# Kernel optimization log

Hardware: AMD Instinct MI355X
Metric: run time of the kernel (lower is better)

Reference implementation:

```python
import jax, jax.numpy as jnp
import numpy as np

B, N, D, H = 256, 1000, 256, 8
DH = D // H
NEG = -1e9
TANH_CLIP = 10.0


def setup_inputs() -> dict:
    key = jax.random.key(0)
    ks = jax.random.split(key, 16)
    f = jax.random.normal
    return {
        "node_embeddings": f(ks[0], (B, N, D), jnp.float32),
        "graph_context": f(ks[1], (B, D), jnp.float32),
        "glimpse_key": f(ks[2], (B, H, N, DH), jnp.float32),
        "glimpse_val": f(ks[3], (B, H, N, DH), jnp.float32),
        "logit_key": f(ks[4], (B, N, D), jnp.float32),
        "capacity": jax.random.uniform(ks[5], (B, 1, 1), jnp.float32),
        "remaining_demand": jax.random.uniform(ks[6], (B, 1, 1), jnp.float32),
        "remaining_nodes": jax.random.uniform(ks[7], (B, 1, 1), jnp.float32),
        "W_ctx": f(ks[8], (2 * D + 3, 2 * D), jnp.float32) / np.sqrt(2 * D + 3),
        "W_out": f(ks[9], (D, D), jnp.float32) / np.sqrt(D),
        "W_sa": f(ks[10], (D, D), jnp.float32) / np.sqrt(D),
        "head": jax.random.randint(ks[11], (B,), 0, N),
        "feasible_nodes": jax.random.randint(ks[12], (B, N), 0, 2, dtype=jnp.int32),
    }


def _mha(q, k, v, mask):
    # q: [B,H,1,DH]; k,v: [B,H,N,DH]; mask: [B,N] True = feasible
    scores = jnp.einsum('bhqd,bhnd->bhqn', q, k) / np.sqrt(DH)
    scores = jnp.where(mask[:, None, None, :], scores, NEG)
    attn = jax.nn.softmax(scores, axis=-1)
    out = jnp.einsum('bhqn,bhnd->bhqd', attn, v)  # [B,H,1,DH]
    return out.transpose(0, 2, 1, 3).reshape(out.shape[0], D)  # [B,D]


def reference(node_embeddings, graph_context, glimpse_key, glimpse_val,
              logit_key, capacity, remaining_demand, remaining_nodes,
              W_ctx, W_out, W_sa, head, feasible_nodes):
    mask = feasible_nodes.astype(bool)
    no_feasible = ~jnp.any(mask, axis=-1)
    mask = mask.at[:, 0].set(mask[:, 0] | no_feasible)  # force node 0 feasible if all masked

    # dynamic features: [B,3]
    dyn = jnp.concatenate([capacity[:, 0], remaining_demand[:, 0], remaining_nodes[:, 0]], axis=-1)
    # current head node embedding via gather_by_index: [B,D]
    cur = jnp.take_along_axis(node_embeddings, head[:, None, None], axis=1)[:, 0]
    step_context = jnp.concatenate([cur, graph_context, dyn], axis=-1) @ W_ctx  # [B,2D]
    glimpse_q, head_in = step_context[:, :D], step_context[:, D:]

    # glimpse multi-head attention (q_len = 1)
    qh = glimpse_q.reshape(B, 1, H, DH).transpose(0, 2, 1, 3)
    glimpse = _mha(qh, glimpse_key, glimpse_val, mask) @ W_out  # [B,D]

    # single-head pointer logits + tanh clip + masking + log-softmax
    logits = jnp.einsum('bd,bnd->bn', glimpse, logit_key) / np.sqrt(D)
    logits = TANH_CLIP * jnp.tanh(logits)
    logits = jnp.where(mask, logits, NEG)
    log_p = jax.nn.log_softmax(logits, axis=-1)  # [B,N]

    # SimpleSetAttention head encoding over the same cached K/V
    qh2 = head_in.reshape(B, 1, H, DH).transpose(0, 2, 1, 3)
    head_encoding = _mha(qh2, glimpse_key, glimpse_val, mask) @ W_sa  # [B,D]
    return log_p, head_encoding
```

## Files before the change

kernel.cpp:

```cpp
#include <hip/hip_runtime.h>
#include <math.h>

#define B 256
#define N 1000
#define D 256
#define H 8
#define DH 32
#define NEG (-1000000000.0f)

__device__ __forceinline__ float waveReduceMax(float v) {
#pragma unroll
    for (int off = 32; off >= 1; off >>= 1) v = fmaxf(v, __shfl_xor(v, off, 64));
    return v;
}
__device__ __forceinline__ float waveReduceSum(float v) {
#pragma unroll
    for (int off = 32; off >= 1; off >>= 1) v += __shfl_xor(v, off, 64);
    return v;
}

__global__ __launch_bounds__(256) void k_mask(
    const int* __restrict__ feas, int* __restrict__ mask_ws)
{
    __shared__ int sRed[4];
    const int b = blockIdx.x;
    const int tid = threadIdx.x;
    int vals[4];
    int orloc = 0;
#pragma unroll
    for (int k = 0; k < 4; ++k) {
        int n = tid + k * 256;
        int v = (n < N) ? feas[b * N + n] : 0;
        vals[k] = v;
        orloc |= v;
    }
#pragma unroll
    for (int off = 32; off >= 1; off >>= 1) orloc |= __shfl_xor(orloc, off, 64);
    if ((tid & 63) == 0) sRed[tid >> 6] = orloc;
    __syncthreads();
    const int anyf = sRed[0] | sRed[1] | sRed[2] | sRed[3];
#pragma unroll
    for (int k = 0; k < 4; ++k) {
        int n = tid + k * 256;
        if (n < N) {
            int m = vals[k];
            if (n == 0 && !anyf) m = 1;
            mask_ws[b * N + n] = m;
        }
    }
}

__global__ __launch_bounds__(256) void k_ctx(
    const float* __restrict__ ne, const float* __restrict__ gc,
    const float* __restrict__ cap, const float* __restrict__ dem,
    const float* __restrict__ rem, const float* __restrict__ Wctx,
    const int* __restrict__ head,
    float* __restrict__ q1_ws, float* __restrict__ q2_ws)
{
    __shared__ float xs[515];
    const int tid = threadIdx.x;
    const int b = blockIdx.x >> 1;
    const int half = blockIdx.x & 1;
    const int hd = head[b];
    for (int i = tid; i < 515; i += 256) {
        float v;
        if (i < 256)       v = ne[(size_t)(b * N + hd) * D + i];
        else if (i < 512)  v = gc[b * D + (i - 256)];
        else if (i == 512) v = cap[b];
        else if (i == 513) v = dem[b];
        else               v = rem[b];
        xs[i] = v;
    }
    __syncthreads();
    const float* __restrict__ wcol = Wctx + half * 256 + tid;
    float a0 = 0.f, a1 = 0.f, a2 = 0.f, a3 = 0.f;
    int i = 0;
#pragma unroll 2
    for (; i + 4 <= 515; i += 4) {
        a0 = fmaf(xs[i + 0], wcol[(i + 0) * 512], a0);
        a1 = fmaf(xs[i + 1], wcol[(i + 1) * 512], a1);
        a2 = fmaf(xs[i + 2], wcol[(i + 2) * 512], a2);
        a3 = fmaf(xs[i + 3], wcol[(i + 3) * 512], a3);
    }
    for (; i < 515; ++i) a0 = fmaf(xs[i], wcol[i * 512], a0);
    float a = (a0 + a1) + (a2 + a3);
    (half ? q2_ws : q1_ws)[b * D + tid] = a;
}

__global__ __launch_bounds__(256) void k_attn(
    const float* __restrict__ gk, const float* __restrict__ gv,
    const float* __restrict__ q1_ws, const float* __restrict__ q2_ws,
    const int* __restrict__ mask_ws,
    float* __restrict__ out1_ws, float* __restrict__ out2_ws)
{
    __shared__ float s1[N];
    __shared__ float s2[N];
    __shared__ float redA[4], redB[4];
    __shared__ __align__(16) float part1[4][DH];
    __shared__ __align__(16) float part2[4][DH];

    const int tid = threadIdx.x;
    const int b = blockIdx.x >> 3;
    const int h = blockIdx.x & 7;
    const int wid = tid >> 6;
    const int lane = tid & 63;
    const int nsub = lane >> 3;
    const int d4 = lane & 7;

    const float4 q1v = ((const float4*)(q1_ws + (size_t)b * D + h * DH))[d4];
    const float4 q2v = ((const float4*)(q2_ws + (size_t)b * D + h * DH))[d4];
    const float scale = 0.17677669529663687f;
    const float4* __restrict__ kb = (const float4*)(gk + (size_t)(b * H + h) * N * DH);
    const int rbase = wid * 32 + nsub;

#pragma unroll 2
    for (int base = 0; base < 896; base += 128) {
        float4 kv[4];
#pragma unroll
        for (int k = 0; k < 4; ++k) kv[k] = kb[(base + rbase + k * 8) * 8 + d4];
#pragma unroll
        for (int k = 0; k < 4; ++k) {
            float d1 = kv[k].x * q1v.x + kv[k].y * q1v.y + kv[k].z * q1v.z + kv[k].w * q1v.w;
            float d2 = kv[k].x * q2v.x + kv[k].y * q2v.y + kv[k].z * q2v.z + kv[k].w * q2v.w;
            d1 += __shfl_xor(d1, 1, 64); d1 += __shfl_xor(d1, 2, 64); d1 += __shfl_xor(d1, 4, 64);
            d2 += __shfl_xor(d2, 1, 64); d2 += __shfl_xor(d2, 2, 64); d2 += __shfl_xor(d2, 4, 64);
            if (d4 == 0) {
                int r = base + rbase + k * 8;
                s1[r] = d1 * scale;
                s2[r] = d2 * scale;
            }
        }
    }
    {
        float4 kv[4];
        int rr[4];
#pragma unroll
        for (int k = 0; k < 4; ++k) {
            rr[k] = 896 + rbase + k * 8;
            kv[k] = (rr[k] < N) ? kb[rr[k] * 8 + d4] : make_float4(0.f, 0.f, 0.f, 0.f);
        }
#pragma unroll
        for (int k = 0; k < 4; ++k) {
            float d1 = kv[k].x * q1v.x + kv[k].y * q1v.y + kv[k].z * q1v.z + kv[k].w * q1v.w;
            float d2 = kv[k].x * q2v.x + kv[k].y * q2v.y + kv[k].z * q2v.z + kv[k].w * q2v.w;
            d1 += __shfl_xor(d1, 1, 64); d1 += __shfl_xor(d1, 2, 64); d1 += __shfl_xor(d1, 4, 64);
            d2 += __shfl_xor(d2, 1, 64); d2 += __shfl_xor(d2, 2, 64); d2 += __shfl_xor(d2, 4, 64);
            if (d4 == 0 && rr[k] < N) {
                s1[rr[k]] = d1 * scale;
                s2[rr[k]] = d2 * scale;
            }
        }
    }
    __syncthreads();

    float m1 = -INFINITY, m2 = -INFINITY;
    float v1[4], v2[4];
#pragma unroll
    for (int k = 0; k < 4; ++k) {
        int n = tid + k * 256;
        if (n < N) {
            int mm = mask_ws[b * N + n];
            v1[k] = mm ? s1[n] : NEG;
            v2[k] = mm ? s2[n] : NEG;
            m1 = fmaxf(m1, v1[k]);
            m2 = fmaxf(m2, v2[k]);
        } else { v1[k] = NEG; v2[k] = NEG; }
    }
    m1 = waveReduceMax(m1);
    m2 = waveReduceMax(m2);
    if ((tid & 63) == 0) { redA[wid] = m1; redB[wid] = m2; }
    __syncthreads();
    m1 = fmaxf(fmaxf(redA[0], redA[1]), fmaxf(redA[2], redA[3]));
    m2 = fmaxf(fmaxf(redB[0], redB[1]), fmaxf(redB[2], redB[3]));
    __syncthreads();

    float sum1 = 0.f, sum2 = 0.f;
#pragma unroll
    for (int k = 0; k < 4; ++k) {
        int n = tid + k * 256;
        if (n < N) {
            float e1 = __expf(v1[k] - m1);
            float e2 = __expf(v2[k] - m2);
            s1[n] = e1; s2[n] = e2;
            sum1 += e1; sum2 += e2;
        }
    }
    sum1 = waveReduceSum(sum1);
    sum2 = waveReduceSum(sum2);
    if ((tid & 63) == 0) { redA[wid] = sum1; redB[wid] = sum2; }
    __syncthreads();
    sum1 = redA[0] + redA[1] + redA[2] + redA[3];
    sum2 = redB[0] + redB[1] + redB[2] + redB[3];

    const float4* __restrict__ vb = (const float4*)(gv + (size_t)(b * H + h) * N * DH);
    float4 a1 = {0.f, 0.f, 0.f, 0.f}, a2 = {0.f, 0.f, 0.f, 0.f};
#pragma unroll 2
    for (int base = 0; base < 896; base += 128) {
        float4 vv[4];
#pragma unroll
        for (int k = 0; k < 4; ++k) vv[k] = vb[(base + rbase + k * 8) * 8 + d4];
#pragma unroll
        for (int k = 0; k < 4; ++k) {
            int r = base + rbase + k * 8;
            float p1 = s1[r], p2 = s2[r];
            a1.x = fmaf(p1, vv[k].x, a1.x); a1.y = fmaf(p1, vv[k].y, a1.y);
            a1.z = fmaf(p1, vv[k].z, a1.z); a1.w = fmaf(p1, vv[k].w, a1.w);
            a2.x = fmaf(p2, vv[k].x, a2.x); a2.y = fmaf(p2, vv[k].y, a2.y);
            a2.z = fmaf(p2, vv[k].z, a2.z); a2.w = fmaf(p2, vv[k].w, a2.w);
        }
    }
    {
        float4 vv[4];
        int rr[4];
#pragma unroll
        for (int k = 0; k < 4; ++k) {
            rr[k] = 896 + rbase + k * 8;
            vv[k] = (rr[k] < N) ? vb[rr[k] * 8 + d4] : make_float4(0.f, 0.f, 0.f, 0.f);
        }
#pragma unroll
        for (int k = 0; k < 4; ++k) {
            float p1 = (rr[k] < N) ? s1[rr[k]] : 0.f;
            float p2 = (rr[k] < N) ? s2[rr[k]] : 0.f;
            a1.x = fmaf(p1, vv[k].x, a1.x); a1.y = fmaf(p1, vv[k].y, a1.y);
            a1.z = fmaf(p1, vv[k].z, a1.z); a1.w = fmaf(p1, vv[k].w, a1.w);
            a2.x = fmaf(p2, vv[k].x, a2.x); a2.y = fmaf(p2, vv[k].y, a2.y);
            a2.z = fmaf(p2, vv[k].z, a2.z); a2.w = fmaf(p2, vv[k].w, a2.w);
        }
    }
#pragma unroll
    for (int off = 8; off <= 32; off <<= 1) {
        a1.x += __shfl_xor(a1.x, off, 64); a1.y += __shfl_xor(a1.y, off, 64);
        a1.z += __shfl_xor(a1.z, off, 64); a1.w += __shfl_xor(a1.w, off, 64);
        a2.x += __shfl_xor(a2.x, off, 64); a2.y += __shfl_xor(a2.y, off, 64);
        a2.z += __shfl_xor(a2.z, off, 64); a2.w += __shfl_xor(a2.w, off, 64);
    }
    if (lane < 8) {
        ((float4*)part1[wid])[d4] = a1;
        ((float4*)part2[wid])[d4] = a2;
    }
    __syncthreads();

    if (tid < 64) {
        int set = tid >> 5, d = tid & 31;
        float tot = set ? (part2[0][d] + part2[1][d] + part2[2][d] + part2[3][d])
                        : (part1[0][d] + part1[1][d] + part1[2][d] + part1[3][d]);
        float rs = 1.f / (set ? sum2 : sum1);
        (set ? out2_ws : out1_ws)[b * D + h * DH + d] = tot * rs;
    }
}

__global__ __launch_bounds__(256) void k_proj(
    const float* __restrict__ out1_ws, const float* __restrict__ out2_ws,
    const float* __restrict__ Wout, const float* __restrict__ Wsa,
    float* __restrict__ glimpse_ws, float* __restrict__ head_enc)
{
    __shared__ float x[D];
    const int tid = threadIdx.x;
    const int b = blockIdx.x >> 1;
    const int which = blockIdx.x & 1;
    const float* __restrict__ src = which ? out2_ws : out1_ws;
    x[tid] = src[b * D + tid];
    __syncthreads();
    const float* __restrict__ W = which ? Wsa : Wout;
    float a = 0.f;
#pragma unroll 8
    for (int i = 0; i < D; ++i) a = fmaf(x[i], W[i * D + tid], a);
    (which ? head_enc : glimpse_ws)[b * D + tid] = a;
}

__global__ __launch_bounds__(256) void k_logits(
    const float* __restrict__ lk, const float* __restrict__ glimpse_ws,
    const int* __restrict__ mask_ws, float* __restrict__ logits_ws)
{
    __shared__ __align__(16) float gsh[D];
    const int tid = threadIdx.x;
    const int b = blockIdx.x >> 2;
    const int chunk = blockIdx.x & 3;
    gsh[tid] = glimpse_ws[b * D + tid];
    __syncthreads();

    const int lane = tid & 63, wid = tid >> 6;
    const float4 gv = ((const float4*)gsh)[lane];
    const int n0 = chunk * 250;
    const int nend = n0 + 250;
    for (int n = n0 + wid * 4; n < nend; n += 16) {
        float4 kr[4];
#pragma unroll
        for (int j = 0; j < 4; ++j) {
            int nn = n + j;
            kr[j] = (nn < nend) ? ((const float4*)(lk + (size_t)(b * N + nn) * D))[lane]
                                : make_float4(0.f, 0.f, 0.f, 0.f);
        }
        float p[4];
#pragma unroll
        for (int j = 0; j < 4; ++j)
            p[j] = kr[j].x * gv.x + kr[j].y * gv.y + kr[j].z * gv.z + kr[j].w * gv.w;
#pragma unroll
        for (int off = 32; off >= 1; off >>= 1) {
#pragma unroll
            for (int j = 0; j < 4; ++j) p[j] += __shfl_xor(p[j], off, 64);
        }
        if (lane == 0) {
#pragma unroll
            for (int j = 0; j < 4; ++j) {
                int nn = n + j;
                if (nn < nend) {
                    float l = 10.0f * tanhf(p[j] * 0.0625f);
                    logits_ws[b * N + nn] = mask_ws[b * N + nn] ? l : NEG;
                }
            }
        }
    }
}

__global__ __launch_bounds__(256) void k_logsoftmax(
    const float* __restrict__ logits_ws, float* __restrict__ logp)
{
    __shared__ float red[4];
    const int tid = threadIdx.x;
    const int b = blockIdx.x;
    float v[4];
    float m = -INFINITY;
#pragma unroll
    for (int k = 0; k < 4; ++k) {
        int n = tid + k * 256;
        v[k] = (n < N) ? logits_ws[b * N + n] : -INFINITY;
        m = fmaxf(m, v[k]);
    }
    m = waveReduceMax(m);
    if ((tid & 63) == 0) red[tid >> 6] = m;
    __syncthreads();
    m = fmaxf(fmaxf(red[0], red[1]), fmaxf(red[2], red[3]));
    __syncthreads();
    float s = 0.f;
#pragma unroll
    for (int k = 0; k < 4; ++k) {
        int n = tid + k * 256;
        if (n < N) s += __expf(v[k] - m);
    }
    s = waveReduceSum(s);
    if ((tid & 63) == 0) red[tid >> 6] = s;
    __syncthreads();
    s = red[0] + red[1] + red[2] + red[3];
    const float lse = m + logf(s);
#pragma unroll
    for (int k = 0; k < 4; ++k) {
        int n = tid + k * 256;
        if (n < N) logp[b * N + n] = v[k] - lse;
    }
}

extern "C" void kernel_launch(void* const* d_in, const int* in_sizes, int n_in,
                              void* d_out, int out_size, void* d_ws, size_t ws_size,
                              hipStream_t stream) {
    const float* ne   = (const float*)d_in[0];
    const float* gc   = (const float*)d_in[1];
    const float* gk   = (const float*)d_in[2];
    const float* gvv  = (const float*)d_in[3];
    const float* lk   = (const float*)d_in[4];
    const float* cap  = (const float*)d_in[5];
    const float* dem  = (const float*)d_in[6];
    const float* rem  = (const float*)d_in[7];
    const float* Wctx = (const float*)d_in[8];
    const float* Wout = (const float*)d_in[9];
    const float* Wsa  = (const float*)d_in[10];
    const int*   head = (const int*)d_in[11];
    const int*   feas = (const int*)d_in[12];
    float* out = (float*)d_out;

    float* ws        = (float*)d_ws;
    float* q1_ws     = ws;
    float* q2_ws     = q1_ws + B * D;
    int*   mask_ws   = (int*)(q2_ws + B * D);
    float* out1_ws   = (float*)(mask_ws + B * N);
    float* out2_ws   = out1_ws + B * D;
    float* glimpse_ws= out2_ws + B * D;
    float* logits_ws = glimpse_ws + B * D;

    hipLaunchKernelGGL(k_mask, dim3(B), dim3(256), 0, stream, feas, mask_ws);
    hipLaunchKernelGGL(k_ctx, dim3(B * 2), dim3(256), 0, stream,
                       ne, gc, cap, dem, rem, Wctx, head, q1_ws, q2_ws);
    hipLaunchKernelGGL(k_attn, dim3(B * H), dim3(256), 0, stream,
                       gk, gvv, q1_ws, q2_ws, mask_ws, out1_ws, out2_ws);
    hipLaunchKernelGGL(k_proj, dim3(B * 2), dim3(256), 0, stream,
                       out1_ws, out2_ws, Wout, Wsa, glimpse_ws, out + B * N);
    hipLaunchKernelGGL(k_logits, dim3(B * 4), dim3(256), 0, stream,
                       lk, glimpse_ws, mask_ws, logits_ws);
    hipLaunchKernelGGL(k_logsoftmax, dim3(B), dim3(256), 0, stream,
                       logits_ws, out);
}
```

Baseline: 831.3 us.

## Use DPP/swizzle reductions and wider per-thread loads in attention and logits kernels

New measurement: 815.0 us. About the same (-2.0%).

```diff
diff --git a/kernel.cpp b/kernel.cpp
--- a/kernel.cpp
+++ b/kernel.cpp
@@ -17,6 +17,22 @@
 #pragma unroll
     for (int off = 32; off >= 1; off >>= 1) v += __shfl_xor(v, off, 64);
     return v;
+}
+
+__device__ __forceinline__ float qxor1_add(float v) {
+    int t = __builtin_amdgcn_update_dpp(0, __float_as_int(v), 0xB1, 0xF, 0xF, true);
+    return v + __int_as_float(t);
+}
+__device__ __forceinline__ float qxor2_add(float v) {
+    int t = __builtin_amdgcn_update_dpp(0, __float_as_int(v), 0x4E, 0xF, 0xF, true);
+    return v + __int_as_float(t);
+}
+__device__ __forceinline__ float sxor4_add(float v) {
+    int t = __builtin_amdgcn_ds_swizzle(__float_as_int(v), 0x101F);
+    return v + __int_as_float(t);
+}
+__device__ __forceinline__ float dot4(float4 a, float4 b) {
+    return a.x * b.x + a.y * b.y + a.z * b.z + a.w * b.w;
 }
 
 __global__ __launch_bounds__(256) void k_mask(
@@ -111,40 +127,40 @@
     const float4 q2v = ((const float4*)(q2_ws + (size_t)b * D + h * DH))[d4];
     const float scale = 0.17677669529663687f;
     const float4* __restrict__ kb = (const float4*)(gk + (size_t)(b * H + h) * N * DH);
-    const int rbase = wid * 32 + nsub;
-
-#pragma unroll 2
-    for (int base = 0; base < 896; base += 128) {
-        float4 kv[4];
-#pragma unroll
-        for (int k = 0; k < 4; ++k) kv[k] = kb[(base + rbase + k * 8) * 8 + d4];
-#pragma unroll
-        for (int k = 0; k < 4; ++k) {
-            float d1 = kv[k].x * q1v.x + kv[k].y * q1v.y + kv[k].z * q1v.z + kv[k].w * q1v.w;
-            float d2 = kv[k].x * q2v.x + kv[k].y * q2v.y + kv[k].z * q2v.z + kv[k].w * q2v.w;
-            d1 += __shfl_xor(d1, 1, 64); d1 += __shfl_xor(d1, 2, 64); d1 += __shfl_xor(d1, 4, 64);
-            d2 += __shfl_xor(d2, 1, 64); d2 += __shfl_xor(d2, 2, 64); d2 += __shfl_xor(d2, 4, 64);
+    const int rb8 = wid * 64 + nsub;
+
+#pragma unroll 1
+    for (int base = 0; base < 768; base += 256) {
+        float4 kv[8];
+#pragma unroll
+        for (int k = 0; k < 8; ++k) kv[k] = kb[(base + rb8 + k * 8) * 8 + d4];
+#pragma unroll
+        for (int k = 0; k < 8; ++k) {
+            float d1 = dot4(kv[k], q1v);
+            float d2 = dot4(kv[k], q2v);
+            d1 = qxor1_add(d1); d1 = qxor2_add(d1); d1 = sxor4_add(d1);
+            d2 = qxor1_add(d2); d2 = qxor2_add(d2); d2 = sxor4_add(d2);
             if (d4 == 0) {
-                int r = base + rbase + k * 8;
+                int r = base + rb8 + k * 8;
                 s1[r] = d1 * scale;
                 s2[r] = d2 * scale;
             }
         }
     }
     {
-        float4 kv[4];
-        int rr[4];
-#pragma unroll
-        for (int k = 0; k < 4; ++k) {
-            rr[k] = 896 + rbase + k * 8;
+        float4 kv[8];
+        int rr[8];
+#pragma unroll
+        for (int k = 0; k < 8; ++k) {
+            rr[k] = 768 + rb8 + k * 8;
             kv[k] = (rr[k] < N) ? kb[rr[k] * 8 + d4] : make_float4(0.f, 0.f, 0.f, 0.f);
         }
 #pragma unroll
-        for (int k = 0; k < 4; ++k) {
-            float d1 = kv[k].x * q1v.x + kv[k].y * q1v.y + kv[k].z * q1v.z + kv[k].w * q1v.w;
-            float d2 = kv[k].x * q2v.x + kv[k].y * q2v.y + kv[k].z * q2v.z + kv[k].w * q2v.w;
-            d1 += __shfl_xor(d1, 1, 64); d1 += __shfl_xor(d1, 2, 64); d1 += __shfl_xor(d1, 4, 64);
-            d2 += __shfl_xor(d2, 1, 64); d2 += __shfl_xor(d2, 2, 64); d2 += __shfl_xor(d2, 4, 64);
+        for (int k = 0; k < 8; ++k) {
+            float d1 = dot4(kv[k], q1v);
+            float d2 = dot4(kv[k], q2v);
+            d1 = qxor1_add(d1); d1 = qxor2_add(d1); d1 = sxor4_add(d1);
+            d2 = qxor1_add(d2); d2 = qxor2_add(d2); d2 = sxor4_add(d2);
             if (d4 == 0 && rr[k] < N) {
                 s1[rr[k]] = d1 * scale;
                 s2[rr[k]] = d2 * scale;
@@ -194,14 +210,14 @@
 
     const float4* __restrict__ vb = (const float4*)(gv + (size_t)(b * H + h) * N * DH);
     float4 a1 = {0.f, 0.f, 0.f, 0.f}, a2 = {0.f, 0.f, 0.f, 0.f};
-#pragma unroll 2
-    for (int base = 0; base < 896; base += 128) {
-        float4 vv[4];
-#pragma unroll
-        for (int k = 0; k < 4; ++k) vv[k] = vb[(base + rbase + k * 8) * 8 + d4];
-#pragma unroll
-        for (int k = 0; k < 4; ++k) {
-            int r = base + rbase + k * 8;
+#pragma unroll 1
+    for (int base = 0; base < 768; base += 256) {
+        float4 vv[8];
+#pragma unroll
+        for (int k = 0; k < 8; ++k) vv[k] = vb[(base + rb8 + k * 8) * 8 + d4];
+#pragma unroll
+        for (int k = 0; k < 8; ++k) {
+            int r = base + rb8 + k * 8;
             float p1 = s1[r], p2 = s2[r];
             a1.x = fmaf(p1, vv[k].x, a1.x); a1.y = fmaf(p1, vv[k].y, a1.y);
             a1.z = fmaf(p1, vv[k].z, a1.z); a1.w = fmaf(p1, vv[k].w, a1.w);
@@ -210,15 +226,15 @@
         }
     }
     {
-        float4 vv[4];
-        int rr[4];
-#pragma unroll
-        for (int k = 0; k < 4; ++k) {
-            rr[k] = 896 + rbase + k * 8;
+        float4 vv[8];
+        int rr[8];
+#pragma unroll
+        for (int k = 0; k < 8; ++k) {
+            rr[k] = 768 + rb8 + k * 8;
             vv[k] = (rr[k] < N) ? vb[rr[k] * 8 + d4] : make_float4(0.f, 0.f, 0.f, 0.f);
         }
 #pragma unroll
-        for (int k = 0; k < 4; ++k) {
+        for (int k = 0; k < 8; ++k) {
             float p1 = (rr[k] < N) ? s1[rr[k]] : 0.f;
             float p2 = (rr[k] < N) ? s2[rr[k]] : 0.f;
             a1.x = fmaf(p1, vv[k].x, a1.x); a1.y = fmaf(p1, vv[k].y, a1.y);
@@ -280,35 +296,32 @@
     __syncthreads();
 
     const int lane = tid & 63, wid = tid >> 6;
-    const float4 gv = ((const float4*)gsh)[lane];
+    const int rs = lane >> 3;
+    const int c  = lane & 7;
+    float4 g[8];
+#pragma unroll
+    for (int j = 0; j < 8; ++j) g[j] = ((const float4*)gsh)[c + 8 * j];
+
     const int n0 = chunk * 250;
     const int nend = n0 + 250;
-    for (int n = n0 + wid * 4; n < nend; n += 16) {
-        float4 kr[4];
-#pragma unroll
-        for (int j = 0; j < 4; ++j) {
-            int nn = n + j;
-            kr[j] = (nn < nend) ? ((const float4*)(lk + (size_t)(b * N + nn) * D))[lane]
-                                : make_float4(0.f, 0.f, 0.f, 0.f);
-        }
-        float p[4];
-#pragma unroll
-        for (int j = 0; j < 4; ++j)
-            p[j] = kr[j].x * gv.x + kr[j].y * gv.y + kr[j].z * gv.z + kr[j].w * gv.w;
-#pragma unroll
-        for (int off = 32; off >= 1; off >>= 1) {
-#pragma unroll
-            for (int j = 0; j < 4; ++j) p[j] += __shfl_xor(p[j], off, 64);
-        }
-        if (lane == 0) {
-#pragma unroll
-            for (int j = 0; j < 4; ++j) {
-                int nn = n + j;
-                if (nn < nend) {
-                    float l = 10.0f * tanhf(p[j] * 0.0625f);
-                    logits_ws[b * N + nn] = mask_ws[b * N + nn] ? l : NEG;
-                }
-            }
+    const float4* __restrict__ lkb = (const float4*)(lk + (size_t)b * N * D);
+
+#pragma unroll 1
+    for (int it = 0; it < 8; ++it) {
+        const int r = n0 + it * 32 + wid * 8 + rs;
+        const bool ok = (r < nend);
+        float4 kv[8];
+#pragma unroll
+        for (int j = 0; j < 8; ++j)
+            kv[j] = ok ? lkb[(size_t)r * 64 + c + 8 * j]
+                       : make_float4(0.f, 0.f, 0.f, 0.f);
+        float p = 0.f;
+#pragma unroll
+        for (int j = 0; j < 8; ++j) p += dot4(kv[j], g[j]);
+        p = qxor1_add(p); p = qxor2_add(p); p = sxor4_add(p);
+        if (c == 0 && ok) {
+            float l = 10.0f * tanhf(p * 0.0625f);
+            logits_ws[b * N + r] = mask_ws[b * N + r] ? l : NEG;
         }
     }
 }
```
